# Performance work log

Hardware: AMD Instinct MI355X
Metric: run time of the kernel (lower is better)

Reference implementation:

```python
import jax, jax.numpy as jnp
import numpy as np

LAMBDA_RECON = 1.0
LAMBDA_IF = 0.5
LAMBDA_SMOOTH = 0.1

B, N, T = 8, 8, 262144


def setup_inputs() -> dict:
    key = jax.random.key(0)
    ks = jax.random.split(key, 7)
    return {
        "recon_real": jax.random.normal(ks[0], (B, T), dtype=jnp.float32),
        "recon_imag": jax.random.normal(ks[1], (B, T), dtype=jnp.float32),
        "target_real": jax.random.normal(ks[2], (B, T), dtype=jnp.float32),
        "target_imag": jax.random.normal(ks[3], (B, T), dtype=jnp.float32),
        "eIF": jax.random.normal(ks[4], (B, N, T), dtype=jnp.float32),
        "target_if": jax.random.normal(ks[5], (B, N, T), dtype=jnp.float32),
        "mode_mask": jax.random.randint(ks[6], (B, N), 0, 2, dtype=jnp.int32),
    }


def _mse(a, b):
    d = a - b
    return jnp.mean(d * d)


def reference(recon_real, recon_imag, target_real, target_imag, eIF, target_if, mode_mask):
    # reconstruction loss: MSE on real part + MSE on imag part
    recon_loss = _mse(recon_real, target_real) + _mse(recon_imag, target_imag)
    total_loss = LAMBDA_RECON * recon_loss

    # IF loss: mask broadcast over time axis, MSE of masked tensors
    maskf = (mode_mask == 1).astype(eIF.dtype)          # [B, N]
    valid = maskf[:, :, None]                            # [B, N, 1] broadcasts over T
    if_loss = _mse(eIF * valid, target_if * valid)
    total_loss = total_loss + LAMBDA_IF * if_loss

    # smoothness: mean of per-(b,n) mean squared temporal diff, over masked modes
    if_diff = eIF[:, :, 1:] - eIF[:, :, :-1]             # [B, N, T-1]
    per_mode = jnp.mean(if_diff * if_diff, axis=-1)      # [B, N]
    count = jnp.sum(maskf)
    smooth_loss = jnp.sum(per_mode * maskf) / jnp.maximum(count, 1.0)
    # original skips smooth term if no mode is active
    smooth_term = jnp.where(count > 0, LAMBDA_SMOOTH * smooth_loss, 0.0)
    total_loss = total_loss + smooth_term

    return total_loss, recon_loss, if_loss, smooth_loss
```

## Files before the change

### kernel.cpp

```cpp
#include <hip/hip_runtime.h>


namespace {
constexpr int    kB = 8;
constexpr int    kN = 8;
constexpr int    kT = 262144;
constexpr long long kBT  = (long long)kB * kT;
constexpr long long kBNT = (long long)kB * kN * kT;

constexpr int THREADS     = 256;
constexpr int GRID        = 2048;
constexpr int RECON_UNITS = 2048;
constexpr int IF_SEGS     = 64;
constexpr int IF_UNITS    = kB * kN * IF_SEGS;

constexpr double LAMBDA_IF     = 0.5;
constexpr double LAMBDA_SMOOTH = 0.1;
}

__device__ __forceinline__ float sq(float x) { return x * x; }

__device__ __forceinline__ void recon_accum(int u, int tid,
                                            const float4* __restrict__ rr4,
                                            const float4* __restrict__ tr4,
                                            const float4* __restrict__ ri4,
                                            const float4* __restrict__ ti4,
                                            float& a0, float& a1) {
    const int v = u * THREADS + tid;
    float4 x = rr4[v], y = tr4[v];
    float4 m = ri4[v], w = ti4[v];
    a0 += sq(x.x - y.x) + sq(x.y - y.y) + sq(x.z - y.z) + sq(x.w - y.w);
    a1 += sq(m.x - w.x) + sq(m.y - w.y) + sq(m.z - w.z) + sq(m.w - w.w);
}

__device__ __forceinline__ void if_accum(int iu, int tid,
                                         const float* __restrict__ eIF,
                                         const float* __restrict__ tIF,
                                         const int* __restrict__ smask,
                                         float& a2, float& a3) {
    const int row = iu >> 6;
    const int seg = iu & (IF_SEGS - 1);
    if (smask[row] != 1) return;

    const float4* e4 = (const float4*)(eIF + (size_t)row * kT);
    const float4* t4 = (const float4*)(tIF + (size_t)row * kT);
    constexpr int VPR = kT / 4;
    const int base = seg * 1024 + tid;
    const int b0 = base, b1 = base + 256, b2 = base + 512, b3 = base + 768;
    const bool lane63 = (tid & 63) == 63;

    float4 e0 = e4[b0], e1 = e4[b1], e2 = e4[b2], e3 = e4[b3];
    float4 q0 = t4[b0], q1 = t4[b1], q2 = t4[b2], q3 = t4[b3];
    float n0 = 0.f, n1 = 0.f, n2 = 0.f, n3 = 0.f;
    if (lane63) {
        n0 = e4[b0 + 1].x;
        n1 = e4[b1 + 1].x;
        n2 = e4[b2 + 1].x;
        n3 = (b3 + 1 < VPR) ? e4[b3 + 1].x : e3.w;
    }
    a2 += sq(e0.x - q0.x) + sq(e0.y - q0.y) + sq(e0.z - q0.z) + sq(e0.w - q0.w)
        + sq(e1.x - q1.x) + sq(e1.y - q1.y) + sq(e1.z - q1.z) + sq(e1.w - q1.w)
        + sq(e2.x - q2.x) + sq(e2.y - q2.y) + sq(e2.z - q2.z) + sq(e2.w - q2.w)
        + sq(e3.x - q3.x) + sq(e3.y - q3.y) + sq(e3.z - q3.z) + sq(e3.w - q3.w);
    a3 += sq(e0.y - e0.x) + sq(e0.z - e0.y) + sq(e0.w - e0.z)
        + sq(e1.y - e1.x) + sq(e1.z - e1.y) + sq(e1.w - e1.z)
        + sq(e2.y - e2.x) + sq(e2.z - e2.y) + sq(e2.w - e2.z)
        + sq(e3.y - e3.x) + sq(e3.z - e3.y) + sq(e3.w - e3.z);
    float s0 = __shfl_down(e0.x, 1, 64);
    float s1 = __shfl_down(e1.x, 1, 64);
    float s2 = __shfl_down(e2.x, 1, 64);
    float s3 = __shfl_down(e3.x, 1, 64);
    if (lane63) { s0 = n0; s1 = n1; s2 = n2; s3 = n3; }
    a3 += sq(s0 - e0.w) + sq(s1 - e1.w) + sq(s2 - e2.w) + sq(s3 - e3.w);
}

__global__ __launch_bounds__(THREADS, 8)
void vncmd_main_kernel(const float* __restrict__ rr, const float* __restrict__ ri,
                       const float* __restrict__ tr, const float* __restrict__ ti,
                       const float* __restrict__ eIF, const float* __restrict__ tIF,
                       const int* __restrict__ mask, double* __restrict__ ws) {
    const int tid = threadIdx.x;
    const int bid = blockIdx.x;

    __shared__ int smask[kB * kN];
    if (tid < kB * kN) smask[tid] = mask[tid];
    __syncthreads();

    float a0 = 0.f, a1 = 0.f, a2 = 0.f, a3 = 0.f;
    recon_accum(bid, tid, (const float4*)rr, (const float4*)tr,
                (const float4*)ri, (const float4*)ti, a0, a1);
    if_accum(bid,        tid, eIF, tIF, smask, a2, a3);
    if_accum(bid + 2048, tid, eIF, tIF, smask, a2, a3);

    double d0 = (double)a0, d1 = (double)a1, d2 = (double)a2, d3 = (double)a3;
    #pragma unroll
    for (int o = 32; o > 0; o >>= 1) {
        d0 += __shfl_down(d0, o, 64);
        d1 += __shfl_down(d1, o, 64);
        d2 += __shfl_down(d2, o, 64);
        d3 += __shfl_down(d3, o, 64);
    }
    __shared__ double lds[4][4];
    const int lane = tid & 63;
    const int wid  = tid >> 6;
    if (lane == 0) { lds[wid][0] = d0; lds[wid][1] = d1; lds[wid][2] = d2; lds[wid][3] = d3; }
    __syncthreads();
    if (tid == 0) {
        double* dst = ws + 4 * bid;
        dst[0] = lds[0][0] + lds[1][0] + lds[2][0] + lds[3][0];
        dst[1] = lds[0][1] + lds[1][1] + lds[2][1] + lds[3][1];
        dst[2] = lds[0][2] + lds[1][2] + lds[2][2] + lds[3][2];
        dst[3] = lds[0][3] + lds[1][3] + lds[2][3] + lds[3][3];
    }
}

__global__ __launch_bounds__(THREADS)
void finalize_kernel(const double* __restrict__ ws,
                     const int* __restrict__ mask,
                     float* __restrict__ out) {
    const int tid = threadIdx.x;
    const double2* w2 = (const double2*)ws;
    double s0 = 0.0, s1 = 0.0, s2 = 0.0, s3 = 0.0;
    #pragma unroll
    for (int k = 0; k < GRID / THREADS; ++k) {
        const int b = k * THREADS + tid;
        double2 p = w2[2 * b], q = w2[2 * b + 1];
        s0 += p.x; s1 += p.y; s2 += q.x; s3 += q.y;
    }
    #pragma unroll
    for (int o = 32; o > 0; o >>= 1) {
        s0 += __shfl_down(s0, o, 64);
        s1 += __shfl_down(s1, o, 64);
        s2 += __shfl_down(s2, o, 64);
        s3 += __shfl_down(s3, o, 64);
    }
    __shared__ double lds[4][4];
    const int lane = tid & 63;
    const int wid  = tid >> 6;
    if (lane == 0) { lds[wid][0] = s0; lds[wid][1] = s1; lds[wid][2] = s2; lds[wid][3] = s3; }
    __syncthreads();
    if (tid == 0) {
        double t0 = lds[0][0] + lds[1][0] + lds[2][0] + lds[3][0];
        double t1 = lds[0][1] + lds[1][1] + lds[2][1] + lds[3][1];
        double t2 = lds[0][2] + lds[1][2] + lds[2][2] + lds[3][2];
        double t3 = lds[0][3] + lds[1][3] + lds[2][3] + lds[3][3];
        int c = 0;
        #pragma unroll
        for (int i = 0; i < kB * kN; ++i) c += (mask[i] == 1);
        double count = (double)c;
        double recon = t0 / (double)kBT + t1 / (double)kBT;
        double ifl   = t2 / (double)kBNT;
        double denom = (count > 1.0 ? count : 1.0) * (double)(kT - 1);
        double smooth = t3 / denom;
        double total = recon + LAMBDA_IF * ifl + (count > 0.0 ? LAMBDA_SMOOTH * smooth : 0.0);
        out[0] = (float)total;
        out[1] = (float)recon;
        out[2] = (float)ifl;
        out[3] = (float)smooth;
    }
}

extern "C" void kernel_launch(void* const* d_in, const int* in_sizes, int n_in,
                              void* d_out, int out_size, void* d_ws, size_t ws_size,
                              hipStream_t stream) {
    const float* rr  = (const float*)d_in[0];
    const float* ri  = (const float*)d_in[1];
    const float* tr  = (const float*)d_in[2];
    const float* ti  = (const float*)d_in[3];
    const float* eIF = (const float*)d_in[4];
    const float* tIF = (const float*)d_in[5];
    const int*   msk = (const int*)d_in[6];
    float* out = (float*)d_out;
    double* ws = (double*)d_ws;

    vncmd_main_kernel<<<GRID, THREADS, 0, stream>>>(
        rr, ri, tr, ti, eIF, tIF, msk, ws);
    finalize_kernel<<<1, THREADS, 0, stream>>>(ws, msk, out);
}
```

Before: 24.82 us.

## Use nontemporal loads, drop mask LDS staging, reduce partials in float

Input streams are now read with nontemporal vector loads, on the reasoning that each element is read once and need not stay in cache. The mask is read straight from global memory in each IF unit, which removes the shared-memory staging and one block barrier. Per-block partials are reduced in float rather than double, and the finalize kernel reads float4 partials with 512 threads. The float partials lose some precision in each block's sum, though the final reduction stays in double.

```diff
diff --git a/kernel.cpp b/kernel.cpp
--- a/kernel.cpp
+++ b/kernel.cpp
@@ -8,27 +8,31 @@
 constexpr long long kBT  = (long long)kB * kT;
 constexpr long long kBNT = (long long)kB * kN * kT;
 
-constexpr int THREADS     = 256;
-constexpr int GRID        = 2048;
-constexpr int RECON_UNITS = 2048;
-constexpr int IF_SEGS     = 64;
-constexpr int IF_UNITS    = kB * kN * IF_SEGS;
+constexpr int THREADS  = 256;
+constexpr int GRID     = 2048;
+constexpr int IF_SEGS  = 64;
 
 constexpr double LAMBDA_IF     = 0.5;
 constexpr double LAMBDA_SMOOTH = 0.1;
 }
 
+typedef float vf4 __attribute__((ext_vector_type(4)));
+
 __device__ __forceinline__ float sq(float x) { return x * x; }
 
+__device__ __forceinline__ vf4 ntld(const vf4* p) {
+    return __builtin_nontemporal_load(p);
+}
+
 __device__ __forceinline__ void recon_accum(int u, int tid,
-                                            const float4* __restrict__ rr4,
-                                            const float4* __restrict__ tr4,
-                                            const float4* __restrict__ ri4,
-                                            const float4* __restrict__ ti4,
+                                            const vf4* __restrict__ rr4,
+                                            const vf4* __restrict__ tr4,
+                                            const vf4* __restrict__ ri4,
+                                            const vf4* __restrict__ ti4,
                                             float& a0, float& a1) {
     const int v = u * THREADS + tid;
-    float4 x = rr4[v], y = tr4[v];
-    float4 m = ri4[v], w = ti4[v];
+    vf4 x = ntld(rr4 + v), y = ntld(tr4 + v);
+    vf4 m = ntld(ri4 + v), w = ntld(ti4 + v);
     a0 += sq(x.x - y.x) + sq(x.y - y.y) + sq(x.z - y.z) + sq(x.w - y.w);
     a1 += sq(m.x - w.x) + sq(m.y - w.y) + sq(m.z - w.z) + sq(m.w - w.w);
 }
@@ -36,23 +40,23 @@
 __device__ __forceinline__ void if_accum(int iu, int tid,
                                          const float* __restrict__ eIF,
                                          const float* __restrict__ tIF,
-                                         const int* __restrict__ smask,
+                                         const int* __restrict__ mask,
                                          float& a2, float& a3) {
     const int row = iu >> 6;
+    if (mask[row] != 1) return;
     const int seg = iu & (IF_SEGS - 1);
-    if (smask[row] != 1) return;
 
-    const float4* e4 = (const float4*)(eIF + (size_t)row * kT);
-    const float4* t4 = (const float4*)(tIF + (size_t)row * kT);
+    const vf4* e4 = (const vf4*)(eIF + (size_t)row * kT);
+    const vf4* t4 = (const vf4*)(tIF + (size_t)row * kT);
     constexpr int VPR = kT / 4;
     const int base = seg * 1024 + tid;
     const int b0 = base, b1 = base + 256, b2 = base + 512, b3 = base + 768;
-    const bool lane63 = (tid & 63) == 63;
+    const bool l63 = ((tid & 63) == 63);
 
-    float4 e0 = e4[b0], e1 = e4[b1], e2 = e4[b2], e3 = e4[b3];
-    float4 q0 = t4[b0], q1 = t4[b1], q2 = t4[b2], q3 = t4[b3];
+    vf4 e0 = ntld(e4 + b0), e1 = ntld(e4 + b1), e2 = ntld(e4 + b2), e3 = ntld(e4 + b3);
+    vf4 q0 = ntld(t4 + b0), q1 = ntld(t4 + b1), q2 = ntld(t4 + b2), q3 = ntld(t4 + b3);
     float n0 = 0.f, n1 = 0.f, n2 = 0.f, n3 = 0.f;
-    if (lane63) {
+    if (l63) {
         n0 = e4[b0 + 1].x;
         n1 = e4[b1 + 1].x;
         n2 = e4[b2 + 1].x;
@@ -70,7 +74,7 @@
     float s1 = __shfl_down(e1.x, 1, 64);
     float s2 = __shfl_down(e2.x, 1, 64);
     float s3 = __shfl_down(e3.x, 1, 64);
-    if (lane63) { s0 = n0; s1 = n1; s2 = n2; s3 = n3; }
+    if (l63) { s0 = n0; s1 = n1; s2 = n2; s3 = n3; }
     a3 += sq(s0 - e0.w) + sq(s1 - e1.w) + sq(s2 - e2.w) + sq(s3 - e3.w);
 }
 
@@ -78,54 +82,52 @@
 void vncmd_main_kernel(const float* __restrict__ rr, const float* __restrict__ ri,
                        const float* __restrict__ tr, const float* __restrict__ ti,
                        const float* __restrict__ eIF, const float* __restrict__ tIF,
-                       const int* __restrict__ mask, double* __restrict__ ws) {
-    const int tid = threadIdx.x;
-    const int bid = blockIdx.x;
-
-    __shared__ int smask[kB * kN];
-    if (tid < kB * kN) smask[tid] = mask[tid];
-    __syncthreads();
+                       const int* __restrict__ mask, float* __restrict__ ws) {
+    const int tid  = threadIdx.x;
+    const int bid  = blockIdx.x;
+    const int lane = tid & 63;
+    const int wid  = tid >> 6;
 
     float a0 = 0.f, a1 = 0.f, a2 = 0.f, a3 = 0.f;
-    recon_accum(bid, tid, (const float4*)rr, (const float4*)tr,
-                (const float4*)ri, (const float4*)ti, a0, a1);
-    if_accum(bid,        tid, eIF, tIF, smask, a2, a3);
-    if_accum(bid + 2048, tid, eIF, tIF, smask, a2, a3);
+    recon_accum(bid, tid, (const vf4*)rr, (const vf4*)tr,
+                (const vf4*)ri, (const vf4*)ti, a0, a1);
+    if_accum(bid,        tid, eIF, tIF, mask, a2, a3);
+    if_accum(bid + 2048, tid, eIF, tIF, mask, a2, a3);
 
-    double d0 = (double)a0, d1 = (double)a1, d2 = (double)a2, d3 = (double)a3;
     #pragma unroll
     for (int o = 32; o > 0; o >>= 1) {
-        d0 += __shfl_down(d0, o, 64);
-        d1 += __shfl_down(d1, o, 64);
-        d2 += __shfl_down(d2, o, 64);
-        d3 += __shfl_down(d3, o, 64);
+        a0 += __shfl_down(a0, o, 64);
+        a1 += __shfl_down(a1, o, 64);
+        a2 += __shfl_down(a2, o, 64);
+        a3 += __shfl_down(a3, o, 64);
     }
-    __shared__ double lds[4][4];
-    const int lane = tid & 63;
-    const int wid  = tid >> 6;
-    if (lane == 0) { lds[wid][0] = d0; lds[wid][1] = d1; lds[wid][2] = d2; lds[wid][3] = d3; }
+    __shared__ float lds[4][4];
+    if (lane == 0) { lds[wid][0] = a0; lds[wid][1] = a1; lds[wid][2] = a2; lds[wid][3] = a3; }
     __syncthreads();
     if (tid == 0) {
-        double* dst = ws + 4 * bid;
-        dst[0] = lds[0][0] + lds[1][0] + lds[2][0] + lds[3][0];
-        dst[1] = lds[0][1] + lds[1][1] + lds[2][1] + lds[3][1];
-        dst[2] = lds[0][2] + lds[1][2] + lds[2][2] + lds[3][2];
-        dst[3] = lds[0][3] + lds[1][3] + lds[2][3] + lds[3][3];
+        vf4 r;
+        r.x = lds[0][0] + lds[1][0] + lds[2][0] + lds[3][0];
+        r.y = lds[0][1] + lds[1][1] + lds[2][1] + lds[3][1];
+        r.z = lds[0][2] + lds[1][2] + lds[2][2] + lds[3][2];
+        r.w = lds[0][3] + lds[1][3] + lds[2][3] + lds[3][3];
+        ((vf4*)ws)[bid] = r;
     }
 }
 
-__global__ __launch_bounds__(THREADS)
-void finalize_kernel(const double* __restrict__ ws,
+__global__ __launch_bounds__(512)
+void finalize_kernel(const float* __restrict__ ws,
                      const int* __restrict__ mask,
                      float* __restrict__ out) {
-    const int tid = threadIdx.x;
-    const double2* w2 = (const double2*)ws;
+    const int tid  = threadIdx.x;
+    const int lane = tid & 63;
+    const int wid  = tid >> 6;
+
+    const vf4* w4 = (const vf4*)ws;
     double s0 = 0.0, s1 = 0.0, s2 = 0.0, s3 = 0.0;
     #pragma unroll
-    for (int k = 0; k < GRID / THREADS; ++k) {
-        const int b = k * THREADS + tid;
-        double2 p = w2[2 * b], q = w2[2 * b + 1];
-        s0 += p.x; s1 += p.y; s2 += q.x; s3 += q.y;
+    for (int k = 0; k < GRID / 512; ++k) {
+        vf4 p = w4[k * 512 + tid];
+        s0 += p.x; s1 += p.y; s2 += p.z; s3 += p.w;
     }
     #pragma unroll
     for (int o = 32; o > 0; o >>= 1) {
@@ -134,16 +136,15 @@
         s2 += __shfl_down(s2, o, 64);
         s3 += __shfl_down(s3, o, 64);
     }
-    __shared__ double lds[4][4];
-    const int lane = tid & 63;
-    const int wid  = tid >> 6;
+    __shared__ double lds[8][4];
     if (lane == 0) { lds[wid][0] = s0; lds[wid][1] = s1; lds[wid][2] = s2; lds[wid][3] = s3; }
     __syncthreads();
     if (tid == 0) {
-        double t0 = lds[0][0] + lds[1][0] + lds[2][0] + lds[3][0];
-        double t1 = lds[0][1] + lds[1][1] + lds[2][1] + lds[3][1];
-        double t2 = lds[0][2] + lds[1][2] + lds[2][2] + lds[3][2];
-        double t3 = lds[0][3] + lds[1][3] + lds[2][3] + lds[3][3];
+        double t0 = 0.0, t1 = 0.0, t2 = 0.0, t3 = 0.0;
+        #pragma unroll
+        for (int i = 0; i < 8; ++i) {
+            t0 += lds[i][0]; t1 += lds[i][1]; t2 += lds[i][2]; t3 += lds[i][3];
+        }
         int c = 0;
         #pragma unroll
         for (int i = 0; i < kB * kN; ++i) c += (mask[i] == 1);
@@ -171,9 +172,9 @@
     const float* tIF = (const float*)d_in[5];
     const int*   msk = (const int*)d_in[6];
     float* out = (float*)d_out;
-    double* ws = (double*)d_ws;
+    float* ws  = (float*)d_ws;
 
     vncmd_main_kernel<<<GRID, THREADS, 0, stream>>>(
         rr, ri, tr, ti, eIF, tIF, msk, ws);
-    finalize_kernel<<<1, THREADS, 0, stream>>>(ws, msk, out);
+    finalize_kernel<<<1, 512, 0, stream>>>(ws, msk, out);
 }
```

After: 22.95 us (median of 2 runs). 1.08x faster.
